# Kernel optimization log

Hardware: AMD Instinct MI355X
Metric: run time of the kernel (lower is better)

## Reference

```python
import jax, jax.numpy as jnp
from jax import lax
import numpy as np

DIM = 256


def setup_inputs() -> dict:
    key = jax.random.key(0)
    ks = jax.random.split(key, 7)
    B, C, H, W = 16, DIM, 64, 64
    s = 0.02
    return {
        "x": jax.random.normal(ks[0], (B, C, H, W), dtype=jnp.float32),
        "qkv_w": jax.random.normal(ks[1], (3 * C, C), dtype=jnp.float32) * s,
        "qkv_b": jnp.zeros((3 * C,), dtype=jnp.float32),
        "proj_w": jax.random.normal(ks[2], (C, C), dtype=jnp.float32) * s,
        "proj_b": jnp.zeros((C,), dtype=jnp.float32),
        "conv_w": jax.random.normal(ks[3], (C, C, 3, 3), dtype=jnp.float32) * s,
        "conv_b": jnp.zeros((C,), dtype=jnp.float32),
    }


def reference(x, qkv_w, qkv_b, proj_w, proj_b, conv_w, conv_b):
    B, C, H, W = x.shape
    N = H * W
    scale = C ** (-0.5)
    # qkv on channels-last tokens: [B,N,3C]
    xp = x.transpose(0, 2, 3, 1).reshape(B, N, C)
    qkv = xp @ qkv_w.T + qkv_b
    q, k, v = jnp.split(qkv, 3, axis=-1)  # each [B,N,C]
    q = q.transpose(0, 2, 1)  # [B,C,N]
    v = v.transpose(0, 2, 1)  # [B,C,N]
    # channel attention: [B,C,C]
    attn = jax.nn.softmax(jnp.einsum('bcn,bnd->bcd', q, k) * scale, axis=-1)
    out = jnp.einsum('bcd,bdn->bcn', attn, v).transpose(0, 2, 1)  # [B,N,C]
    out = out @ proj_w.T + proj_b  # [B,N,C]
    # faithful to original: direct reshape [B,N,C] -> [B,C,H,W]
    attn_out = out.reshape(B, C, H, W)
    conv_out = lax.conv_general_dilated(
        x, conv_w, window_strides=(1, 1), padding=[(1, 1), (1, 1)],
        dimension_numbers=('NCHW', 'OIHW', 'NCHW'))
    conv_out = conv_out + conv_b[None, :, None, None]
    return attn_out + conv_out
```

## Files before the change

### kernel.cpp

```cpp
#include <hip/hip_runtime.h>
#include <hip/hip_bf16.h>

typedef unsigned short u16;
typedef __bf16 bf16x8 __attribute__((ext_vector_type(8)));
typedef float f32x4 __attribute__((ext_vector_type(4)));

#define BATCH 16
#define C 256
#define NTOK 4096
#define CN 1048576

__device__ __forceinline__ u16 f2b(float f) {
  __hip_bfloat16 h = __float2bfloat16(f);
  return __builtin_bit_cast(u16, h);
}
__device__ __forceinline__ float b2f(u16 u) {
  unsigned int x = ((unsigned int)u) << 16;
  return __builtin_bit_cast(float, x);
}

__device__ __forceinline__ void glds16(const u16* g, u16* l) {
  __builtin_amdgcn_global_load_lds(
      (const __attribute__((address_space(1))) unsigned int*)(g),
      (__attribute__((address_space(3))) unsigned int*)(l), 16, 0, 0);
}

__global__ __launch_bounds__(256) void prep_kernel(
    const float* __restrict__ x, const float* __restrict__ qkv_w,
    const float* __restrict__ proj_w, const float* __restrict__ conv_w,
    u16* __restrict__ xbf, u16* __restrict__ xT, float* __restrict__ rws,
    u16* __restrict__ WqT, u16* __restrict__ Wk, u16* __restrict__ WvT,
    u16* __restrict__ Pw, u16* __restrict__ cw) {
  __shared__ float t[32][33];
  int bx = blockIdx.x;
  int tid = threadIdx.x;
  if (bx < 16384) {
    int n0 = (bx & 127) * 32;
    int c0 = ((bx >> 7) & 7) * 32;
    int b = bx >> 10;
    int i = tid >> 3, j4 = (tid & 7) * 4;
    const float* xb = x + (long)b * CN;
    float4 v = *(const float4*)(xb + (long)(c0 + i) * NTOK + n0 + j4);
    ushort4 bv;
    bv.x = f2b(v.x); bv.y = f2b(v.y); bv.z = f2b(v.z); bv.w = f2b(v.w);
    *(ushort4*)(xbf + (long)b * CN + (long)(c0 + i) * NTOK + n0 + j4) = bv;
    t[i][j4 + 0] = v.x; t[i][j4 + 1] = v.y; t[i][j4 + 2] = v.z; t[i][j4 + 3] = v.w;
    __syncthreads();
    ushort4 o;
    o.x = f2b(t[j4 + 0][i]); o.y = f2b(t[j4 + 1][i]);
    o.z = f2b(t[j4 + 2][i]); o.w = f2b(t[j4 + 3][i]);
    *(ushort4*)(xT + (long)b * CN + (long)(n0 + i) * C + c0 + j4) = o;
    if (tid < 32) {
      float s = 0.f;
#pragma unroll
      for (int j = 0; j < 32; ++j) s += t[tid][j];
      atomicAdd(&rws[b * C + c0 + tid], s);
    }
  } else {
    int idx = (bx - 16384) * 256 + tid;
    if (idx < 65536) {
      WqT[(idx & 255) * 256 + (idx >> 8)] = f2b(qkv_w[idx]);
    } else if (idx < 131072) {
      int e = idx - 65536;
      Wk[e] = f2b(qkv_w[65536 + e]);
    } else if (idx < 196608) {
      int e = idx - 131072;
      int i = e >> 8, d = e & 255;
      WvT[e] = f2b(qkv_w[131072 + d * 256 + i]);
    } else if (idx < 262144) {
      int e = idx - 196608;
      Pw[e] = f2b(proj_w[e]);
    } else if (idx < 851968) {
      int e = idx - 262144;
      int o = e / 2304;
      int rem = e - o * 2304;
      int tap = rem >> 8, i = rem & 255;
      cw[e] = f2b(conv_w[o * 2304 + i * 9 + tap]);
    }
  }
}

template <int EPI>
__global__ __launch_bounds__(256, 2) void gemm_glds_kernel(
    const u16* __restrict__ A, const u16* __restrict__ B, void* __restrict__ Cv,
    int K, int lda, int ldb, int ldc, int tilesN, long sA, long sB, long sC) {
  int b = blockIdx.z, ks = blockIdx.y;
  A += (long)b * sA + (long)ks * K;
  B += (long)b * sB + (long)ks * K;
  int ty = blockIdx.x / tilesN, tx = blockIdx.x % tilesN;
  int row0 = ty * 128, col0 = tx * 128;

  __shared__ u16 lA[2][4096];
  __shared__ u16 lB[2][4096];

  int tid = threadIdx.x;
  int lane = tid & 63, wv = tid >> 6;
  int wm = wv >> 1, wn = wv & 1;
  int fr = lane & 15, kq = lane >> 4;
  int kqs = kq ^ ((fr >> 1) & 3);

  int c0 = wv * 128 + lane, c1 = c0 + 64;
  int r0s = c0 >> 2, r1s = c1 >> 2;
  int ls0 = (c0 & 3) ^ ((r0s >> 1) & 3);
  int ls1 = (c1 & 3) ^ ((r1s >> 1) & 3);
  const u16* pA0 = A + (long)(row0 + r0s) * lda + ls0 * 8;
  const u16* pA1 = A + (long)(row0 + r1s) * lda + ls1 * 8;
  const u16* pB0 = B + (long)(col0 + r0s) * ldb + ls0 * 8;
  const u16* pB1 = B + (long)(col0 + r1s) * ldb + ls1 * 8;
  int dst0 = wv * 1024, dst1 = wv * 1024 + 512;

  f32x4 acc[4][4] = {};

  auto STAGE = [&](int buf, int t) {
    int k0 = t << 5;
    glds16(pA0 + k0, &lA[buf][dst0]);
    glds16(pA1 + k0, &lA[buf][dst1]);
    glds16(pB0 + k0, &lB[buf][dst0]);
    glds16(pB1 + k0, &lB[buf][dst1]);
  };
  auto COMPUTE = [&](int buf) {
    bf16x8 af[4], bfr[4];
#pragma unroll
    for (int m = 0; m < 4; ++m)
      af[m] = *(const bf16x8*)&lA[buf][(wm * 64 + m * 16 + fr) * 32 + kqs * 8];
#pragma unroll
    for (int n = 0; n < 4; ++n)
      bfr[n] = *(const bf16x8*)&lB[buf][(wn * 64 + n * 16 + fr) * 32 + kqs * 8];
#pragma unroll
    for (int m = 0; m < 4; ++m)
#pragma unroll
      for (int n = 0; n < 4; ++n)
        acc[m][n] = __builtin_amdgcn_mfma_f32_16x16x32_bf16(af[m], bfr[n], acc[m][n], 0, 0, 0);
  };

  int nk = K >> 5, cur = 0;
  STAGE(0, 0);
  __syncthreads();
  for (int t = 0; t < nk; ++t) {
    if (t + 1 < nk) STAGE(cur ^ 1, t + 1);
    COMPUTE(cur);
    __syncthreads();
    cur ^= 1;
  }

  if (EPI == 5) {
    __hip_bfloat16* Cb =
        (__hip_bfloat16*)Cv + ((long)b * gridDim.y + ks) * sC;
#pragma unroll
    for (int m = 0; m < 4; ++m)
#pragma unroll
      for (int n = 0; n < 4; ++n)
#pragma unroll
        for (int r = 0; r < 4; ++r) {
          int gr = row0 + wm * 64 + m * 16 + kq * 4 + r;
          int gc = col0 + wn * 64 + n * 16 + fr;
          Cb[(long)gr * ldc + gc] = __float2bfloat16(acc[m][n][r]);
        }
  }
}

template <int EPI>
__global__ __launch_bounds__(256, 2) void gemm64_kernel(
    const u16* __restrict__ A, const u16* __restrict__ B, void* __restrict__ Cv,
    long sA, long sB, long sC, const float* __restrict__ e1,
    const float* __restrict__ e2, const float* __restrict__ e4) {
  if (EPI == 4 && blockIdx.x == 16) {
    int bb = blockIdx.z, j = threadIdx.x;
    const u16* m = A + (long)bb * sA + (long)j * 256;
    float s = 0.f;
    for (int d = 0; d < 256; ++d) s += b2f(m[d]) * e1[512 + d];
    float* cbout = const_cast<float*>(e4);
    cbout[bb * 256 + j] = e2[j] + s;
    return;
  }
  int b = blockIdx.z;
  A += (long)b * sA;
  B += (long)b * sB;
  int ty = blockIdx.x >> 2, tx = blockIdx.x & 3;
  int row0 = ty * 64, col0 = tx * 64;

  __shared__ u16 lA[2][2048];
  __shared__ u16 lB[2][2048];

  int tid = threadIdx.x;
  int lane = tid & 63, w = tid >> 6;
  int wm = w >> 1, wn = w & 1;
  int fr = lane & 15, kq = lane >> 4;
  int kqs = kq ^ ((fr >> 1) & 3);

  int rs = tid >> 2;
  int ls = (tid & 3) ^ ((rs >> 1) & 3);
  const u16* pA = A + (long)(row0 + rs) * 256 + ls * 8;
  const u16* pB = B + (long)(col0 + rs) * 256 + ls * 8;
  int dst = w * 512;

  f32x4 acc[2][2] = {};

  auto STAGE = [&](int buf, int t) {
    int k0 = t << 5;
    glds16(pA + k0, &lA[buf][dst]);
    glds16(pB + k0, &lB[buf][dst]);
  };
  auto COMPUTE = [&](int buf) {
    bf16x8 af[2], bfr[2];
#pragma unroll
    for (int m = 0; m < 2; ++m)
      af[m] = *(const bf16x8*)&lA[buf][(wm * 32 + m * 16 + fr) * 32 + kqs * 8];
#pragma unroll
    for (int n = 0; n < 2; ++n)
      bfr[n] = *(const bf16x8*)&lB[buf][(wn * 32 + n * 16 + fr) * 32 + kqs * 8];
#pragma unroll
    for (int m = 0; m < 2; ++m)
#pragma unroll
      for (int n = 0; n < 2; ++n)
        acc[m][n] = __builtin_amdgcn_mfma_f32_16x16x32_bf16(af[m], bfr[n], acc[m][n], 0, 0, 0);
  };

  int cur = 0;
  STAGE(0, 0);
  __syncthreads();
  for (int t = 0; t < 8; ++t) {
    if (t + 1 < 8) STAGE(cur ^ 1, t + 1);
    COMPUTE(cur);
    __syncthreads();
    cur ^= 1;
  }

  __hip_bfloat16* Cb = (__hip_bfloat16*)Cv + (long)b * sC;
#pragma unroll
  for (int m = 0; m < 2; ++m)
#pragma unroll
    for (int n = 0; n < 2; ++n)
#pragma unroll
      for (int r = 0; r < 4; ++r) {
        int gr = row0 + wm * 32 + m * 16 + kq * 4 + r;
        int gc = col0 + wn * 32 + n * 16 + fr;
        Cb[(long)gr * 256 + gc] = __float2bfloat16(acc[m][n][r]);
      }
}

__global__ __launch_bounds__(256, 2) void s_softmax_kernel(
    const u16* __restrict__ T1, const u16* __restrict__ Wk,
    u16* __restrict__ attnT, const float* __restrict__ qkv_b,
    const float* __restrict__ uws, const float* __restrict__ wws) {
  int b = blockIdx.y;
  int r0 = blockIdx.x * 32;
  const u16* Ab = T1 + (long)b * 65536 + (long)r0 * 256;

  __shared__ u16 lA[2][1024];
  __shared__ u16 lB[2][8192];
  __shared__ float sf[32][257];
  __shared__ float red[32][8];
  __shared__ float rmax[32], rinv[32];

  int tid = threadIdx.x;
  int lane = tid & 63, w = tid >> 6;
  int fr = lane & 15, kq = lane >> 4;
  int kqs = kq ^ ((fr >> 1) & 3);

  int rsA = tid >> 2;
  int lsA = (tid & 3) ^ ((rsA >> 1) & 3);
  const u16* pA = Ab + (long)rsA * 256 + lsA * 8;
  int lrB = lane >> 2;
  int lsB = (lane & 3) ^ ((lrB >> 1) & 3);
  const u16* pB = Wk + (long)(w * 64 + lrB) * 256 + lsB * 8;

  f32x4 acc[2][4] = {};

  auto STAGE = [&](int buf, int t) {
    int k0 = t << 5;
    if (w == 0) glds16(pA + k0, &lA[buf][0]);
    if (w == 1) glds16(pA + k0, &lA[buf][512]);
    glds16(pB + k0, &lB[buf][(w * 64 + 0) * 32]);
    glds16(pB + 16 * 256 + k0, &lB[buf][(w * 64 + 16) * 32]);
    glds16(pB + 32 * 256 + k0, &lB[buf][(w * 64 + 32) * 32]);
    glds16(pB + 48 * 256 + k0, &lB[buf][(w * 64 + 48) * 32]);
  };
  auto COMPUTE = [&](int buf) {
    bf16x8 af[2], bfr[4];
#pragma unroll
    for (int m = 0; m < 2; ++m)
      af[m] = *(const bf16x8*)&lA[buf][(m * 16 + fr) * 32 + kqs * 8];
#pragma unroll
    for (int n = 0; n < 4; ++n)
      bfr[n] = *(const bf16x8*)&lB[buf][(w * 64 + n * 16 + fr) * 32 + kqs * 8];
#pragma unroll
    for (int m = 0; m < 2; ++m)
#pragma unroll
      for (int n = 0; n < 4; ++n)
        acc[m][n] = __builtin_amdgcn_mfma_f32_16x16x32_bf16(af[m], bfr[n], acc[m][n], 0, 0, 0);
  };

  int cur = 0;
  STAGE(0, 0);
  __syncthreads();
  for (int t = 0; t < 8; ++t) {
    if (t + 1 < 8) STAGE(cur ^ 1, t + 1);
    COMPUTE(cur);
    __syncthreads();
    cur ^= 1;
  }

  const float* ub = uws + b * 256;
  const float* wb = wws + b * 256;
#pragma unroll
  for (int m = 0; m < 2; ++m)
#pragma unroll
    for (int n = 0; n < 4; ++n)
#pragma unroll
      for (int r = 0; r < 4; ++r) {
        int row = m * 16 + kq * 4 + r;
        int col = w * 64 + n * 16 + fr;
        float qb = qkv_b[r0 + row];
        float v = acc[m][n][r] + qb * ub[col] + qkv_b[256 + col] * wb[r0 + row] +
                  4096.0f * qb * qkv_b[256 + col];
        sf[row][col] = v * 0.0625f;
      }
  __syncthreads();

  int rr = tid >> 3, sg = (tid & 7) * 32;
  float mx = -3.4e38f;
  for (int c2 = sg; c2 < sg + 32; ++c2) mx = fmaxf(mx, sf[rr][c2]);
  red[rr][tid & 7] = mx;
  __syncthreads();
  if (tid < 32) {
    float m2 = red[tid][0];
#pragma unroll
    for (int k = 1; k < 8; ++k) m2 = fmaxf(m2, red[tid][k]);
    rmax[tid] = m2;
  }
  __syncthreads();
  float m2 = rmax[rr], sm = 0.f;
  for (int c2 = sg; c2 < sg + 32; ++c2) {
    float e = __expf(sf[rr][c2] - m2);
    sf[rr][c2] = e;
    sm += e;
  }
  red[rr][tid & 7] = sm;
  __syncthreads();
  if (tid < 32) {
    float s2 = red[tid][0];
#pragma unroll
    for (int k = 1; k < 8; ++k) s2 += red[tid][k];
    rinv[tid] = 1.0f / s2;
  }
  __syncthreads();
  int c = tid;
  u16* aT = attnT + (long)b * 65536 + (long)c * 256 + r0;
#pragma unroll 8
  for (int r = 0; r < 32; ++r) aT[r] = f2b(sf[r][c] * rinv[r]);
}

__global__ __launch_bounds__(256) void reduceG_T1_bias_kernel(
    const u16* __restrict__ Gp, const u16* __restrict__ WqT,
    u16* __restrict__ T1, const float* __restrict__ qkv_w,
    const float* __restrict__ r, float* __restrict__ u, float* __restrict__ w) {
  int b = blockIdx.y;
  if (blockIdx.x < 64) {
    __shared__ float g[4][256];
    int tid = threadIdx.x;
    int e = blockIdx.x * 1024 + tid * 4;
    const u16* base = Gp + (long)b * 8 * 65536;
    float s0 = 0.f, s1 = 0.f, s2 = 0.f, s3 = 0.f;
#pragma unroll
    for (int sl = 0; sl < 8; ++sl) {
      ushort4 v = *(const ushort4*)(base + (long)sl * 65536 + e);
      s0 += b2f(v.x); s1 += b2f(v.y); s2 += b2f(v.z); s3 += b2f(v.w);
    }
    int rr = tid >> 6, cc = (tid & 63) * 4;
    g[rr][cc + 0] = s0; g[rr][cc + 1] = s1;
    g[rr][cc + 2] = s2; g[rr][cc + 3] = s3;
    __syncthreads();
    int c = tid;
    float a0 = 0.f, a1 = 0.f, a2 = 0.f, a3 = 0.f;
#pragma unroll 4
    for (int i = 0; i < 256; ++i) {
      float wq = b2f(WqT[i * 256 + c]);
      a0 += wq * g[0][i]; a1 += wq * g[1][i];
      a2 += wq * g[2][i]; a3 += wq * g[3][i];
    }
    ushort4 o;
    o.x = f2b(a0); o.y = f2b(a1); o.z = f2b(a2); o.w = f2b(a3);
    *(ushort4*)(T1 + (long)b * 65536 + (long)c * 256 + blockIdx.x * 4) = o;
  } else {
    int t = threadIdx.x;
    const float* rb = r + b * C;
    float su = 0.f, sw = 0.f;
    for (int i = 0; i < C; ++i) {
      float rv = rb[i];
      su += qkv_w[(256 + t) * 256 + i] * rv;
      sw += qkv_w[t * 256 + i] * rv;
    }
    u[b * C + t] = su;
    w[b * C + t] = sw;
  }
}

__global__ __launch_bounds__(256, 2) void convattn_kernel(
    const u16* __restrict__ xT, const u16* __restrict__ cw,
    const u16* __restrict__ W2, const u16* __restrict__ zbuf,
    const float* __restrict__ conv_b, const float* __restrict__ cb,
    float* __restrict__ out) {
  int b = blockIdx.y;
  int to = blockIdx.x >> 5;
  int tn = blockIdx.x & 31;
  int row0 = to * 128, col0 = tn * 128;
  const u16* xTb = xT + (long)b * CN;
  const u16* W2b = W2 + (long)b * 65536;

  __shared__ u16 lA[2][8192];
  __shared__ u16 lB[2][8192];

  int tid = threadIdx.x;
  int lane = tid & 63, w = tid >> 6;
  int wm = w >> 1, wn = w & 1;
  int fr = lane & 15, kq = lane >> 4;
  int fx = fr & 7;

  int lr = lane >> 3, sl = lane & 7;
  int ss = sl ^ lr;

  const u16* aA[4]; const u16* pBt[4]; int hh[4], ww[4];
  const u16* zsrc = zbuf + ss * 8;
#pragma unroll
  for (int i = 0; i < 4; ++i) {
    int r = w * 32 + i * 8 + lr;
    aA[i] = cw + (long)(row0 + r) * 2304 + ss * 8;
    int t = col0 + r;
    hh[i] = t >> 6; ww[i] = t & 63;
    pBt[i] = xTb + (long)t * 256 + ss * 8;
  }
  int nb = col0 >> 8, jb = col0 & 255;

  f32x4 acc[4][4] = {};
  const u16 *at0, *at1, *at2, *at3, *bt0, *bt1, *bt2, *bt3;

  auto set_tap = [&](int tap) {
    int dh = tap / 3 - 1, dw = tap % 3 - 1;
    long sh = (long)(dh * 64 + dw) * 256;
    at0 = aA[0] + tap * 256; at1 = aA[1] + tap * 256;
    at2 = aA[2] + tap * 256; at3 = aA[3] + tap * 256;
    bool v0 = ((unsigned)(hh[0] + dh) < 64u) && ((unsigned)(ww[0] + dw) < 64u);
    bool v1 = ((unsigned)(hh[1] + dh) < 64u) && ((unsigned)(ww[1] + dw) < 64u);
    bool v2 = ((unsigned)(hh[2] + dh) < 64u) && ((unsigned)(ww[2] + dw) < 64u);
    bool v3 = ((unsigned)(hh[3] + dh) < 64u) && ((unsigned)(ww[3] + dw) < 64u);
    bt0 = v0 ? pBt[0] + sh : zsrc;
    bt1 = v1 ? pBt[1] + sh : zsrc;
    bt2 = v2 ? pBt[2] + sh : zsrc;
    bt3 = v3 ? pBt[3] + sh : zsrc;
  };
  auto set_attn = [&]() {
#pragma unroll
    for (int i = 0; i < 4; ++i) {
      int r = w * 32 + i * 8 + lr;
      const u16* a = xTb + (long)((row0 + r) * 16 + nb) * 256 + ss * 8;
      const u16* bb = W2b + (long)(jb + r) * 256 + ss * 8;
      if (i == 0) { at0 = a; bt0 = bb; }
      else if (i == 1) { at1 = a; bt1 = bb; }
      else if (i == 2) { at2 = a; bt2 = bb; }
      else { at3 = a; bt3 = bb; }
    }
  };

  auto STAGE = [&](int buf, int chunk) {
    int k = chunk * 64;
    glds16(at0 + k, &lA[buf][(w * 32 + 0) * 64]);
    glds16(at1 + k, &lA[buf][(w * 32 + 8) * 64]);
    glds16(at2 + k, &lA[buf][(w * 32 + 16) * 64]);
    glds16(at3 + k, &lA[buf][(w * 32 + 24) * 64]);
    glds16(bt0 + k, &lB[buf][(w * 32 + 0) * 64]);
    glds16(bt1 + k, &lB[buf][(w * 32 + 8) * 64]);
    glds16(bt2 + k, &lB[buf][(w * 32 + 16) * 64]);
    glds16(bt3 + k, &lB[buf][(w * 32 + 24) * 64]);
  };
  auto COMPUTE = [&](int buf) {
    bf16x8 af[4][2], bf[4][2];
#pragma unroll
    for (int m = 0; m < 4; ++m) {
      int row = wm * 64 + m * 16 + fr;
#pragma unroll
      for (int kh = 0; kh < 2; ++kh)
        af[m][kh] = *(const bf16x8*)&lA[buf][row * 64 + (((kh << 2) + kq) ^ fx) * 8];
    }
#pragma unroll
    for (int n = 0; n < 4; ++n) {
      int row = wn * 64 + n * 16 + fr;
#pragma unroll
      for (int kh = 0; kh < 2; ++kh)
        bf[n][kh] = *(const bf16x8*)&lB[buf][row * 64 + (((kh << 2) + kq) ^ fx) * 8];
    }
    __builtin_amdgcn_s_setprio(1);
#pragma unroll
    for (int kh = 0; kh < 2; ++kh)
#pragma unroll
      for (int m = 0; m < 4; ++m)
#pragma unroll
        for (int n = 0; n < 4; ++n)
          acc[m][n] = __builtin_amdgcn_mfma_f32_16x16x32_bf16(af[m][kh], bf[n][kh], acc[m][n], 0, 0, 0);
    __builtin_amdgcn_s_setprio(0);
  };

  set_tap(0);
  STAGE(0, 0);
  asm volatile("s_waitcnt vmcnt(0)" ::: "memory");
  __builtin_amdgcn_sched_barrier(0);
  __builtin_amdgcn_s_barrier();
  __builtin_amdgcn_sched_barrier(0);

  int buf = 0;
#pragma unroll 1
  for (int T = 0; T < 10; ++T) {
#pragma unroll
    for (int j = 0; j < 4; ++j) {
      if (!(T == 9 && j == 3)) {
        if (j < 3) {
          STAGE(buf ^ 1, j + 1);
        } else {
          if (T < 8) set_tap(T + 1);
          else set_attn();
          STAGE(buf ^ 1, 0);
        }
      }
      COMPUTE(buf);
      asm volatile("s_waitcnt vmcnt(0)" ::: "memory");
      __builtin_amdgcn_sched_barrier(0);
      __builtin_amdgcn_s_barrier();
      __builtin_amdgcn_sched_barrier(0);
      buf ^= 1;
    }
  }

  float* ob = out + (long)b * CN;
  const float* cbb = cb + b * C;
#pragma unroll
  for (int m = 0; m < 4; ++m) {
    int go = row0 + wm * 64 + m * 16 + kq * 4;
#pragma unroll
    for (int nn = 0; nn < 4; ++nn) {
      int cc = wn * 64 + nn * 16 + fr;
      float cbv = cbb[jb + cc];
#pragma unroll
      for (int r = 0; r < 4; ++r)
        ob[(long)(go + r) * NTOK + col0 + cc] =
            acc[m][nn][r] + conv_b[go + r] + cbv;
    }
  }
}

extern "C" void kernel_launch(void* const* d_in, const int* in_sizes, int n_in,
                              void* d_out, int out_size, void* d_ws, size_t ws_size,
                              hipStream_t stream) {
  const float* x = (const float*)d_in[0];
  const float* qkv_w = (const float*)d_in[1];
  const float* qkv_b = (const float*)d_in[2];
  const float* proj_w = (const float*)d_in[3];
  const float* proj_b = (const float*)d_in[4];
  const float* conv_w = (const float*)d_in[5];
  const float* conv_b = (const float*)d_in[6];
  float* out = (float*)d_out;
  char* ws = (char*)d_ws;

  u16* xbf = (u16*)(ws);
  u16* xT = (u16*)(ws + 33554432);
  u16* T1bf = (u16*)(ws + 67108864);
  u16* Gpart = (u16*)(ws + 69206016);
  u16* attnT = (u16*)(ws + 75497472);
  u16* Mbf = (u16*)(ws + 77594624);
  u16* W2bf = (u16*)(ws + 79691776);
  u16* WqT = (u16*)(ws + 85983232);
  u16* Wk = (u16*)(ws + 86114304);
  u16* WvT = (u16*)(ws + 86245376);
  u16* Pw = (u16*)(ws + 86376448);
  u16* cw = (u16*)(ws + 86507520);
  float* rws = (float*)(ws + 87687168);
  u16* zbuf = (u16*)(ws + 87703552);
  float* uws = (float*)(ws + 87704064);
  float* wws = (float*)(ws + 87720448);
  float* cb = (float*)(ws + 87736832);

  hipMemsetAsync(ws + 87687168, 0, 16896, stream);

  prep_kernel<<<19712, 256, 0, stream>>>(x, qkv_w, proj_w, conv_w, xbf, xT,
                                         rws, WqT, Wk, WvT, Pw, cw);

  gemm_glds_kernel<5><<<dim3(4, 8, BATCH), 256, 0, stream>>>(
      xbf, xbf, Gpart, 512, 4096, 4096, 256, 2, CN, CN, 65536);
  reduceG_T1_bias_kernel<<<dim3(65, BATCH), 256, 0, stream>>>(
      Gpart, WqT, T1bf, qkv_w, rws, uws, wws);

  s_softmax_kernel<<<dim3(8, BATCH), 256, 0, stream>>>(
      T1bf, Wk, attnT, qkv_b, uws, wws);

  gemm64_kernel<1><<<dim3(16, 1, BATCH), 256, 0, stream>>>(
      Pw, attnT, Mbf, 0, 65536, 65536, nullptr, nullptr, nullptr);
  gemm64_kernel<4><<<dim3(17, 1, BATCH), 256, 0, stream>>>(
      Mbf, WvT, W2bf, 65536, 0, 65536, qkv_b, proj_b, cb);

  convattn_kernel<<<dim3(64, BATCH), 256, 0, stream>>>(xT, cw, W2bf, zbuf,
                                                       conv_b, cb, out);
}
```

Measured before the change: 204.5 us.

## Fuse two chained small GEMMs and bias reduction into one kernel

Replaces the two gemm64 launches (Pw·attn then M·Wv plus a bias block) with one kernel. Each block computes a 64-row strip of the intermediate M, keeps it in LDS as bf16, computes the bias row sums from it, then multiplies it by WvT to produce W2. This removes one launch and the global round-trip of M. In exchange the grid shrinks from 256+ blocks to 64 larger blocks, which lowers parallelism, and LDS use per block grows.

```diff
diff --git a/kernel.cpp b/kernel.cpp
--- a/kernel.cpp
+++ b/kernel.cpp
@@ -159,83 +159,122 @@
   }
 }
 
-template <int EPI>
-__global__ __launch_bounds__(256, 2) void gemm64_kernel(
-    const u16* __restrict__ A, const u16* __restrict__ B, void* __restrict__ Cv,
-    long sA, long sB, long sC, const float* __restrict__ e1,
-    const float* __restrict__ e2, const float* __restrict__ e4) {
-  if (EPI == 4 && blockIdx.x == 16) {
-    int bb = blockIdx.z, j = threadIdx.x;
-    const u16* m = A + (long)bb * sA + (long)j * 256;
-    float s = 0.f;
-    for (int d = 0; d < 256; ++d) s += b2f(m[d]) * e1[512 + d];
-    float* cbout = const_cast<float*>(e4);
-    cbout[bb * 256 + j] = e2[j] + s;
-    return;
-  }
-  int b = blockIdx.z;
-  A += (long)b * sA;
-  B += (long)b * sB;
-  int ty = blockIdx.x >> 2, tx = blockIdx.x & 3;
-  int row0 = ty * 64, col0 = tx * 64;
+__global__ __launch_bounds__(256, 2) void mw2_kernel(
+    const u16* __restrict__ Pw, const u16* __restrict__ attnT,
+    const u16* __restrict__ WvT, u16* __restrict__ W2,
+    const float* __restrict__ qkv_b, const float* __restrict__ proj_b,
+    float* __restrict__ cb) {
+  int b = blockIdx.y;
+  int r0 = blockIdx.x * 64;
+  const u16* aTb = attnT + (long)b * 65536;
 
   __shared__ u16 lA[2][2048];
-  __shared__ u16 lB[2][2048];
+  __shared__ u16 lB[2][8192];
+  __shared__ u16 mts[64][264];
+  __shared__ float cred[64][4];
 
   int tid = threadIdx.x;
   int lane = tid & 63, w = tid >> 6;
-  int wm = w >> 1, wn = w & 1;
   int fr = lane & 15, kq = lane >> 4;
   int kqs = kq ^ ((fr >> 1) & 3);
 
-  int rs = tid >> 2;
-  int ls = (tid & 3) ^ ((rs >> 1) & 3);
-  const u16* pA = A + (long)(row0 + rs) * 256 + ls * 8;
-  const u16* pB = B + (long)(col0 + rs) * 256 + ls * 8;
-  int dst = w * 512;
-
-  f32x4 acc[2][2] = {};
-
-  auto STAGE = [&](int buf, int t) {
+  int rsA = tid >> 2;
+  int lsA = (tid & 3) ^ ((rsA >> 1) & 3);
+  const u16* pA = Pw + (long)(r0 + rsA) * 256 + lsA * 8;
+  int lrB = lane >> 2;
+  int lsB = (lane & 3) ^ ((lrB >> 1) & 3);
+  long boff = (long)(w * 64 + lrB) * 256 + lsB * 8;
+
+  f32x4 acc[4][4] = {};
+
+  auto STAGE = [&](const u16* Bsrc, int buf, int t) {
     int k0 = t << 5;
-    glds16(pA + k0, &lA[buf][dst]);
-    glds16(pB + k0, &lB[buf][dst]);
-  };
-  auto COMPUTE = [&](int buf) {
-    bf16x8 af[2], bfr[2];
-#pragma unroll
-    for (int m = 0; m < 2; ++m)
-      af[m] = *(const bf16x8*)&lA[buf][(wm * 32 + m * 16 + fr) * 32 + kqs * 8];
-#pragma unroll
-    for (int n = 0; n < 2; ++n)
-      bfr[n] = *(const bf16x8*)&lB[buf][(wn * 32 + n * 16 + fr) * 32 + kqs * 8];
-#pragma unroll
-    for (int m = 0; m < 2; ++m)
-#pragma unroll
-      for (int n = 0; n < 2; ++n)
+    glds16(pA + k0, &lA[buf][w * 512]);
+#pragma unroll
+    for (int i = 0; i < 4; ++i)
+      glds16(Bsrc + boff + i * 4096 + k0, &lB[buf][(w * 64 + i * 16) * 32]);
+  };
+  auto COMPUTE1 = [&](int buf) {
+    bf16x8 af[4], bfr[4];
+#pragma unroll
+    for (int m = 0; m < 4; ++m)
+      af[m] = *(const bf16x8*)&lA[buf][(m * 16 + fr) * 32 + kqs * 8];
+#pragma unroll
+    for (int n = 0; n < 4; ++n)
+      bfr[n] = *(const bf16x8*)&lB[buf][(w * 64 + n * 16 + fr) * 32 + kqs * 8];
+#pragma unroll
+    for (int m = 0; m < 4; ++m)
+#pragma unroll
+      for (int n = 0; n < 4; ++n)
         acc[m][n] = __builtin_amdgcn_mfma_f32_16x16x32_bf16(af[m], bfr[n], acc[m][n], 0, 0, 0);
   };
 
   int cur = 0;
-  STAGE(0, 0);
+  STAGE(aTb, 0, 0);
   __syncthreads();
   for (int t = 0; t < 8; ++t) {
-    if (t + 1 < 8) STAGE(cur ^ 1, t + 1);
-    COMPUTE(cur);
+    if (t + 1 < 8) STAGE(aTb, cur ^ 1, t + 1);
+    COMPUTE1(cur);
     __syncthreads();
     cur ^= 1;
   }
-
-  __hip_bfloat16* Cb = (__hip_bfloat16*)Cv + (long)b * sC;
-#pragma unroll
-  for (int m = 0; m < 2; ++m)
-#pragma unroll
-    for (int n = 0; n < 2; ++n)
+#pragma unroll
+  for (int m = 0; m < 4; ++m)
+#pragma unroll
+    for (int n = 0; n < 4; ++n)
+#pragma unroll
+      for (int r = 0; r < 4; ++r)
+        mts[m * 16 + kq * 4 + r][w * 64 + n * 16 + fr] = f2b(acc[m][n][r]);
+  __syncthreads();
+
+  cur = 0;
+  STAGE(WvT, 0, 0);
+  {
+    int j = tid >> 2, q = tid & 3;
+    float s = 0.f;
+    int d0 = q * 64;
+#pragma unroll 8
+    for (int d = d0; d < d0 + 64; ++d) s += b2f(mts[j][d]) * qkv_b[512 + d];
+    cred[j][q] = s;
+  }
+  __syncthreads();
+  if (tid < 64)
+    cb[b * 256 + r0 + tid] = proj_b[r0 + tid] +
+        cred[tid][0] + cred[tid][1] + cred[tid][2] + cred[tid][3];
+
+#pragma unroll
+  for (int m = 0; m < 4; ++m)
+#pragma unroll
+    for (int n = 0; n < 4; ++n)
+      acc[m][n] = f32x4{0.f, 0.f, 0.f, 0.f};
+  for (int t = 0; t < 8; ++t) {
+    if (t + 1 < 8) STAGE(WvT, cur ^ 1, t + 1);
+    bf16x8 af[4], bfr[4];
+#pragma unroll
+    for (int m = 0; m < 4; ++m)
+      af[m] = *(const bf16x8*)&mts[m * 16 + fr][t * 32 + kq * 8];
+#pragma unroll
+    for (int n = 0; n < 4; ++n)
+      bfr[n] = *(const bf16x8*)&lB[cur][(w * 64 + n * 16 + fr) * 32 + kqs * 8];
+#pragma unroll
+    for (int m = 0; m < 4; ++m)
+#pragma unroll
+      for (int n = 0; n < 4; ++n)
+        acc[m][n] = __builtin_amdgcn_mfma_f32_16x16x32_bf16(af[m], bfr[n], acc[m][n], 0, 0, 0);
+    __syncthreads();
+    cur ^= 1;
+  }
+
+  __hip_bfloat16* W2b = (__hip_bfloat16*)W2 + (long)b * 65536;
+#pragma unroll
+  for (int m = 0; m < 4; ++m)
+#pragma unroll
+    for (int n = 0; n < 4; ++n)
 #pragma unroll
       for (int r = 0; r < 4; ++r) {
-        int gr = row0 + wm * 32 + m * 16 + kq * 4 + r;
-        int gc = col0 + wn * 32 + n * 16 + fr;
-        Cb[(long)gr * 256 + gc] = __float2bfloat16(acc[m][n][r]);
+        int gr = r0 + m * 16 + kq * 4 + r;
+        int gc = w * 64 + n * 16 + fr;
+        W2b[(long)gr * 256 + gc] = __float2bfloat16(acc[m][n][r]);
       }
 }
 
@@ -565,7 +604,6 @@
   u16* T1bf = (u16*)(ws + 67108864);
   u16* Gpart = (u16*)(ws + 69206016);
   u16* attnT = (u16*)(ws + 75497472);
-  u16* Mbf = (u16*)(ws + 77594624);
   u16* W2bf = (u16*)(ws + 79691776);
   u16* WqT = (u16*)(ws + 85983232);
   u16* Wk = (u16*)(ws + 86114304);
@@ -591,10 +629,8 @@
   s_softmax_kernel<<<dim3(8, BATCH), 256, 0, stream>>>(
       T1bf, Wk, attnT, qkv_b, uws, wws);
 
-  gemm64_kernel<1><<<dim3(16, 1, BATCH), 256, 0, stream>>>(
-      Pw, attnT, Mbf, 0, 65536, 65536, nullptr, nullptr, nullptr);
-  gemm64_kernel<4><<<dim3(17, 1, BATCH), 256, 0, stream>>>(
-      Mbf, WvT, W2bf, 65536, 0, 65536, qkv_b, proj_b, cb);
+  mw2_kernel<<<dim3(4, BATCH), 256, 0, stream>>>(
+      Pw, attnT, WvT, W2bf, qkv_b, proj_b, cb);
 
   convattn_kernel<<<dim3(64, BATCH), 256, 0, stream>>>(xT, cw, W2bf, zbuf,
                                                        conv_b, cb, out);
```

New measurement: 203.3 us. About the same (-0.6%).
